# Performance work log

Hardware: AMD Instinct MI355X
Metric: run time of the kernel (lower is better)

## Reference

```python
import jax, jax.numpy as jnp
import numpy as np

HEADS, DIM_HEAD, DIM = 8, 64, 512
INNER = HEADS * DIM_HEAD  # 512


def setup_inputs() -> dict:
    key = jax.random.key(0)
    k1, k2, k3 = jax.random.split(key, 3)
    b, n = 2, 2048
    x = jax.random.normal(k1, (b, n, DIM), dtype=jnp.float32)
    # to_qkv: Linear(dim, 4*inner_dim, bias=False); weight stored [out, in]
    w_qkv = jax.random.normal(k2, (4 * INNER, DIM), dtype=jnp.float32) * (1.0 / np.sqrt(DIM))
    # to_out: Linear(2*inner_dim, dim) with bias
    w_out = jax.random.normal(k3, (DIM, 2 * INNER), dtype=jnp.float32) * (1.0 / np.sqrt(2 * INNER))
    b_out = jnp.zeros((DIM,), dtype=jnp.float32)
    return {"x": x, "w_qkv": w_qkv, "w_out": w_out, "b_out": b_out}


def reference(x, w_qkv, w_out, b_out):
    b, n, d = x.shape
    qkvt = x @ w_qkv.T  # [b, n, 4*inner]
    q, k, v, t = jnp.split(qkvt, 4, axis=-1)

    def split_heads(z):
        return z.reshape(b, n, HEADS, DIM_HEAD).transpose(0, 2, 1, 3)  # [b,h,n,dh]

    q, k, v, t = map(split_heads, (q, k, v, t))

    scale = DIM_HEAD ** -0.5
    dots = jnp.einsum('bhid,bhjd->bhij', q, k) * scale
    attn1 = jax.nn.softmax(dots, axis=-1)

    # fixed positional-decay attention: exp(-|i-j|/e), torch broadcast-normalized
    idx = jnp.arange(1, n + 1, dtype=x.dtype)  # linspace(1, n, n)
    tg = jnp.abs(idx[None, :] - idx[:, None])  # [n, n]
    a2 = jnp.exp(-tg / jnp.exp(jnp.asarray(1.0, x.dtype)))
    a2 = a2 / a2.sum(-1)  # broadcasts over last axis, as in the torch code

    out1 = jnp.einsum('bhij,bhjd->bhid', attn1, v)
    out2 = jnp.einsum('ij,bhjd->bhid', a2, t)
    out = jnp.concatenate([out1, out2], axis=-1)  # [b,h,n,2*dh]
    out = out.transpose(0, 2, 1, 3).reshape(b, n, HEADS * 2 * DIM_HEAD)  # [b,n,2*inner]
    return out @ w_out.T + b_out
```

## Files before the change

### kernel.cpp

```cpp
#include <hip/hip_runtime.h>
#include <hip/hip_bf16.h>
#include <stdint.h>

typedef unsigned short u16;
typedef __bf16 bf16;
typedef __bf16 bf16x8 __attribute__((ext_vector_type(8)));
typedef float f32x4 __attribute__((ext_vector_type(4)));
typedef float f32x16 __attribute__((ext_vector_type(16)));

#define NSEQ 2048
#define NDH 64
#define NH 8
#define QKS 2097152ull

__device__ __forceinline__ float b2f(u16 u) {
  union { float f; uint32_t i; } x; x.i = ((uint32_t)u) << 16; return x.f;
}
__device__ __forceinline__ u16 f2b(float f) {
  union { float f; uint32_t i; } x; x.f = f;
  const uint32_t r = x.i + 0x7FFFu + ((x.i >> 16) & 1u);
  return (u16)(r >> 16);
}
__device__ __forceinline__ uint32_t b2pk(float a, float b) {
  union { __hip_bfloat162 h; uint32_t u; } x;
  x.h = __float22bfloat162_rn(make_float2(a, b));
  return x.u;
}
__device__ __forceinline__ void gl16(const void* g, void* l) {
  __builtin_amdgcn_global_load_lds(
      (const __attribute__((address_space(1))) void*)g,
      (__attribute__((address_space(3))) void*)l, 16, 0, 0);
}

__global__ __launch_bounds__(256) void k_cvt(
    const float* __restrict__ X, const float* __restrict__ Wq,
    const float* __restrict__ Wo, u16* __restrict__ Xb,
    u16* __restrict__ Wqb, u16* __restrict__ Wob) {
  const int b = blockIdx.x;
  const float* src; u16* dst; int idx;
  if (b < 1024)      { src = X;  dst = Xb;  idx = b; }
  else if (b < 1536) { src = Wq; dst = Wqb; idx = b - 1024; }
  else               { src = Wo; dst = Wob; idx = b - 1536; }
  const size_t off = ((size_t)idx * 256 + threadIdx.x) * 8;
  const float4 a = *(const float4*)(src + off);
  const float4 c = *(const float4*)(src + off + 4);
  uint4 o = {b2pk(a.x, a.y), b2pk(a.z, a.w), b2pk(c.x, c.y), b2pk(c.z, c.w)};
  *(uint4*)(dst + off) = o;
}

__global__ __launch_bounds__(256) void k_gemm_qkvt(
    const u16* __restrict__ Xb, const u16* __restrict__ Wb, u16* __restrict__ qkvt) {
  __shared__ __align__(16) bf16 smem[18432];
  bf16* A0e = smem;
  bf16* A1e = smem + 4096;
  bf16* B0e = smem + 8192;
  bf16* B1e = smem + 12288;
  const int tid = threadIdx.x;
  const int m0 = blockIdx.x * 128;
  const int n0 = blockIdx.y * 128;
  const int w = tid >> 6, lane = tid & 63;
  const int wy = w >> 1, wx = w & 1;
  const int quad = lane >> 4, l15 = lane & 15;
  const int srow = tid >> 2, sc8 = (tid & 3) * 8;
  const u16* ag = Xb + (size_t)(m0 + srow) * 512 + sc8;
  const u16* bg = Wb + (size_t)(n0 + srow) * 512 + sc8;
  char* aL00 = (char*)smem + w * 1024;
  char* aL01 = (char*)smem + 4096  + w * 1024;
  char* aL10 = (char*)smem + 8192  + w * 1024;
  char* aL11 = (char*)smem + 12288 + w * 1024;
  char* bL00 = (char*)smem + 16384 + w * 1024;
  char* bL01 = (char*)smem + 20480 + w * 1024;
  char* bL10 = (char*)smem + 24576 + w * 1024;
  char* bL11 = (char*)smem + 28672 + w * 1024;
  f32x4 acc[4][4];
#pragma unroll
  for (int mt = 0; mt < 4; ++mt)
#pragma unroll
    for (int nt = 0; nt < 4; ++nt) acc[mt][nt] = (f32x4){0.f, 0.f, 0.f, 0.f};
  for (int kc = 0; kc < 512; kc += 64) {
    __syncthreads();
    gl16(ag + kc,                 aL00);
    gl16(ag + kc + 64 * 512,      aL01);
    gl16(ag + kc + 32,            aL10);
    gl16(ag + kc + 32 + 64 * 512, aL11);
    gl16(bg + kc,                 bL00);
    gl16(bg + kc + 64 * 512,      bL01);
    gl16(bg + kc + 32,            bL10);
    gl16(bg + kc + 32 + 64 * 512, bL11);
    __syncthreads();
#pragma unroll
    for (int ks = 0; ks < 2; ++ks) {
      const bf16* Ae = ks ? A1e : A0e;
      const bf16* Be = ks ? B1e : B0e;
      bf16x8 afr[4], bfr[4];
#pragma unroll
      for (int mt = 0; mt < 4; ++mt)
        afr[mt] = *(const bf16x8*)&Ae[(wy * 64 + mt * 16 + l15) * 32 + quad * 8];
#pragma unroll
      for (int nt = 0; nt < 4; ++nt)
        bfr[nt] = *(const bf16x8*)&Be[(wx * 64 + nt * 16 + l15) * 32 + quad * 8];
#pragma unroll
      for (int mt = 0; mt < 4; ++mt)
#pragma unroll
        for (int nt = 0; nt < 4; ++nt)
          acc[mt][nt] = __builtin_amdgcn_mfma_f32_16x16x32_bf16(afr[mt], bfr[nt], acc[mt][nt], 0, 0, 0);
    }
  }
  __syncthreads();
  const int cbase = n0 + wx * 64;
  const int which = cbase >> 9;
  const int h     = (cbase >> 6) & 7;
  const float scale = (which == 0) ? 0.18033688011112043f : 1.0f;
  bf16* Cw = smem + w * 4608;
  if (which == 2) {
#pragma unroll
    for (int nt = 0; nt < 4; ++nt)
#pragma unroll
      for (int mt = 0; mt < 4; ++mt)
#pragma unroll
        for (int r = 0; r < 4; ++r)
          Cw[(nt * 16 + l15) * 72 + mt * 16 + quad * 4 + r] = (bf16)acc[mt][nt][r];
  } else {
#pragma unroll
    for (int mt = 0; mt < 4; ++mt)
#pragma unroll
      for (int nt = 0; nt < 4; ++nt)
#pragma unroll
        for (int r = 0; r < 4; ++r)
          Cw[(mt * 16 + quad * 4 + r) * 72 + nt * 16 + l15] = (bf16)(acc[mt][nt][r] * scale);
  }
  const int mb = m0 + wy * 64;
  const int bb = mb >> 11;
  const int nn0 = mb & (NSEQ - 1);
  if (which == 2) {
    u16* vt = qkvt + 2ull * QKS + (size_t)(bb * NH + h) * NDH * NSEQ;
#pragma unroll
    for (int p = 0; p < 8; ++p) {
      const int d = p * 8 + (lane >> 3);
      const int t8 = (lane & 7) * 8;
      const uint4 v = *(const uint4*)&Cw[d * 72 + t8];
      *(uint4*)(vt + (size_t)d * NSEQ + nn0 + t8) = v;
    }
  } else {
    u16* dst = qkvt + (size_t)which * QKS + ((size_t)(bb * NH + h) * NSEQ + nn0) * NDH;
#pragma unroll
    for (int p = 0; p < 8; ++p) {
      const int tok = p * 8 + (lane >> 3);
      const int c8 = (lane & 7) * 8;
      const uint4 v = *(const uint4*)&Cw[tok * 72 + c8];
      *(uint4*)(dst + (size_t)tok * NDH + c8) = v;
    }
  }
}

__global__ __launch_bounds__(256) void k_attn(
    const u16* __restrict__ qkvt, u16* __restrict__ out12) {
  __shared__ float Os[4][32][64];
  __shared__ float Lp[4][32];
  const int tid = threadIdx.x;
  const int bid = blockIdx.x;
  const int bh = bid & 15;
  const int qt = bid >> 4;
  const size_t base  = (size_t)bh * (NSEQ * NDH);
  const size_t vbase = 2ull * QKS + (size_t)bh * (NDH * NSEQ);
  const int wq = tid >> 6, lane = tid & 63;
  const int l31 = lane & 31, hi = lane >> 5;
  const u16* qp = qkvt + base + (size_t)(qt * 32 + l31) * NDH + hi * 8;
  bf16x8 qb[4];
#pragma unroll
  for (int c = 0; c < 4; ++c) qb[c] = *(const bf16x8*)(qp + c * 16);
  const u16* kp = qkvt + QKS + base + (size_t)(wq * 512 + l31) * NDH + hi * 8;
  const u16* vp = qkvt + vbase + (size_t)wq * 512 + hi * 8;
  float lacc = 0.f;
  f32x16 o[2];
#pragma unroll
  for (int nt = 0; nt < 2; ++nt)
#pragma unroll
    for (int r = 0; r < 16; ++r) o[nt][r] = 0.f;
  bf16x8 kf[4];
#pragma unroll
  for (int c = 0; c < 4; ++c) kf[c] = *(const bf16x8*)(kp + c * 16);
  for (int t = 0; t < 16; ++t) {
    bf16x8 vf[2][2];
#pragma unroll
    for (int nt = 0; nt < 2; ++nt)
#pragma unroll
      for (int c = 0; c < 2; ++c)
        vf[nt][c] = *(const bf16x8*)(vp + (size_t)(nt * 32 + l31) * NSEQ + t * 32 + c * 16);
    f32x16 s;
#pragma unroll
    for (int r = 0; r < 16; ++r) s[r] = 0.f;
    __builtin_amdgcn_s_setprio(1);
#pragma unroll
    for (int c = 0; c < 4; ++c)
      s = __builtin_amdgcn_mfma_f32_32x32x16_bf16(kf[c], qb[c], s, 0, 0, 0);
    __builtin_amdgcn_s_setprio(0);
    const int tn = (t + 1) & 15;
    bf16x8 kfn[4];
#pragma unroll
    for (int c = 0; c < 4; ++c)
      kfn[c] = *(const bf16x8*)(kp + (size_t)tn * 32 * NDH + c * 16);
    float ts = 0.f;
#pragma unroll
    for (int r = 0; r < 16; ++r) {
      s[r] = __builtin_amdgcn_exp2f(s[r]);
      ts += s[r];
    }
    ts += __shfl_xor(ts, 32);
    lacc += ts;
    const uint32_t w0 = b2pk(s[0], s[1]),   w1 = b2pk(s[2], s[3]);
    const uint32_t w2 = b2pk(s[4], s[5]),   w3 = b2pk(s[6], s[7]);
    const uint32_t w4 = b2pk(s[8], s[9]),   w5 = b2pk(s[10], s[11]);
    const uint32_t w6 = b2pk(s[12], s[13]), w7 = b2pk(s[14], s[15]);
    const uint32_t e0 = __shfl_xor(hi ? w0 : w2, 32);
    const uint32_t e1 = __shfl_xor(hi ? w1 : w3, 32);
    const uint32_t e2 = __shfl_xor(hi ? w4 : w6, 32);
    const uint32_t e3 = __shfl_xor(hi ? w5 : w7, 32);
    uint4 u0 = hi ? (uint4){e0, e1, w2, w3} : (uint4){w0, w1, e0, e1};
    uint4 u1 = hi ? (uint4){e2, e3, w6, w7} : (uint4){w4, w5, e2, e3};
    const bf16x8 pa0 = *(const bf16x8*)&u0;
    const bf16x8 pa1 = *(const bf16x8*)&u1;
    __builtin_amdgcn_s_setprio(1);
    o[0] = __builtin_amdgcn_mfma_f32_32x32x16_bf16(pa0, vf[0][0], o[0], 0, 0, 0);
    o[0] = __builtin_amdgcn_mfma_f32_32x32x16_bf16(pa1, vf[0][1], o[0], 0, 0, 0);
    o[1] = __builtin_amdgcn_mfma_f32_32x32x16_bf16(pa0, vf[1][0], o[1], 0, 0, 0);
    o[1] = __builtin_amdgcn_mfma_f32_32x32x16_bf16(pa1, vf[1][1], o[1], 0, 0, 0);
    __builtin_amdgcn_s_setprio(0);
#pragma unroll
    for (int c = 0; c < 4; ++c) kf[c] = kfn[c];
  }
#pragma unroll
  for (int nt = 0; nt < 2; ++nt)
#pragma unroll
    for (int r = 0; r < 16; ++r) {
      const int row = (r & 3) + 8 * (r >> 2) + 4 * hi;
      Os[wq][row][nt * 32 + l31] = o[nt][r];
    }
  if (lane < 32) Lp[wq][lane] = lacc;
  __syncthreads();
  const int bb = bh >> 3, h = bh & 7;
#pragma unroll
  for (int rr = 0; rr < 8; ++rr) {
    const int row = wq * 8 + rr;
    const float lt = Lp[0][row] + Lp[1][row] + Lp[2][row] + Lp[3][row];
    const float inv = 1.f / lt;
    const float sum = Os[0][row][lane] + Os[1][row][lane] +
                      Os[2][row][lane] + Os[3][row][lane];
    out12[(size_t)(bb * NSEQ + qt * 32 + row) * 1024 + h * 128 + lane] =
        f2b(sum * inv);
  }
}

__global__ __launch_bounds__(256) void k_band(
    const u16* __restrict__ qkvt, u16* __restrict__ out12) {
  __shared__ float sinv[4][192];
  __shared__ float fbuf[4][64][68];
  const int tid = threadIdx.x;
  const int w = tid >> 6, d = tid & 63;
  const int c  = blockIdx.x * 4 + w;
  const int i0 = c * 64;
  const int bh = blockIdx.y;
  const size_t tb = 3ull * QKS + (size_t)bh * (NSEQ * NDH);
  const float EI = 0.36787944117144233f;
  const float RR = 0.69220062755534635f;
  const float OMR = 1.f - RR;
#pragma unroll
  for (int p = 0; p < 3; ++p) {
    const int j = i0 - 64 + p * 64 + d;
    const float r1 = __expf(-(float)(j + 1) * EI);
    const float r2 = __expf(-(float)(NSEQ - j) * EI);
    sinv[w][p * 64 + d] = OMR / (1.f - r1 + RR - r2);
  }
  const u16* tp = qkvt + tb + d;
  float f = 0.f;
  if (c > 0) {
#pragma unroll 8
    for (int jj = 0; jj < 64; ++jj)
      f = RR * f + sinv[w][jj] * b2f(tp[(size_t)(i0 - 64 + jj) * NDH]);
  }
#pragma unroll 8
  for (int jj = 0; jj < 64; ++jj) {
    f = RR * f + sinv[w][64 + jj] * b2f(tp[(size_t)(i0 + jj) * NDH]);
    fbuf[w][jj][d] = f;
  }
  float b = 0.f;
  if (c < 31) {
#pragma unroll 8
    for (int jj = 63; jj >= 0; --jj)
      b = RR * b + sinv[w][128 + jj] * b2f(tp[(size_t)(i0 + 64 + jj) * NDH]);
  }
  const int bb = bh >> 3, h = bh & 7;
#pragma unroll 8
  for (int jj = 63; jj >= 0; --jj) {
    const float g = sinv[w][64 + jj] * b2f(tp[(size_t)(i0 + jj) * NDH]);
    b = RR * b + g;
    out12[(size_t)(bb * NSEQ + i0 + jj) * 1024 + h * 128 + 64 + d] =
        f2b(fbuf[w][jj][d] + b - g);
  }
}

__global__ __launch_bounds__(256) void k_gemm_out(
    const u16* __restrict__ A, const u16* __restrict__ Wb,
    const float* __restrict__ bias, float* __restrict__ out) {
  __shared__ __align__(16) float smemf[6144];
  bf16* A0e = (bf16*)smemf;
  bf16* A1e = (bf16*)smemf + 4096;
  bf16* B0e = (bf16*)smemf + 8192;
  bf16* B1e = (bf16*)smemf + 10240;
  const int tid = threadIdx.x;
  const int m0 = blockIdx.x * 128;
  const int n0 = blockIdx.y * 64;
  const int w = tid >> 6, lane = tid & 63;
  const int wy = w >> 1, wx = w & 1;
  const int quad = lane >> 4, l15 = lane & 15;
  const int srow = tid >> 2, sc8 = (tid & 3) * 8;
  const u16* ap = A  + (size_t)(m0 + srow) * 1024 + sc8;
  const u16* bp = Wb + (size_t)(n0 + srow) * 1024 + sc8;
  char* aL00 = (char*)smemf + w * 1024;
  char* aL01 = (char*)smemf + 4096  + w * 1024;
  char* aL10 = (char*)smemf + 8192  + w * 1024;
  char* aL11 = (char*)smemf + 12288 + w * 1024;
  char* bL0  = (char*)smemf + 16384 + w * 1024;
  char* bL1  = (char*)smemf + 20480 + w * 1024;
  f32x4 acc[4][2];
#pragma unroll
  for (int mt = 0; mt < 4; ++mt)
#pragma unroll
    for (int nt = 0; nt < 2; ++nt) acc[mt][nt] = (f32x4){0.f, 0.f, 0.f, 0.f};
  for (int kc = 0; kc < 1024; kc += 64) {
    __syncthreads();
    gl16(ap + kc,                  aL00);
    gl16(ap + kc + 64 * 1024,      aL01);
    gl16(ap + kc + 32,             aL10);
    gl16(ap + kc + 32 + 64 * 1024, aL11);
    gl16(bp + kc,                  bL0);
    gl16(bp + kc + 32,             bL1);
    __syncthreads();
#pragma unroll
    for (int ks = 0; ks < 2; ++ks) {
      const bf16* Ae = ks ? A1e : A0e;
      const bf16* Be = ks ? B1e : B0e;
      bf16x8 afr[4], bfr[2];
#pragma unroll
      for (int mt = 0; mt < 4; ++mt)
        afr[mt] = *(const bf16x8*)&Ae[(wy * 64 + mt * 16 + l15) * 32 + quad * 8];
#pragma unroll
      for (int nt = 0; nt < 2; ++nt)
        bfr[nt] = *(const bf16x8*)&Be[(wx * 32 + nt * 16 + l15) * 32 + quad * 8];
#pragma unroll
      for (int mt = 0; mt < 4; ++mt)
#pragma unroll
        for (int nt = 0; nt < 2; ++nt)
          acc[mt][nt] = __builtin_amdgcn_mfma_f32_16x16x32_bf16(afr[mt], bfr[nt], acc[mt][nt], 0, 0, 0);
    }
  }
  float bias_v[2];
#pragma unroll
  for (int nt = 0; nt < 2; ++nt) bias_v[nt] = bias[n0 + wx * 32 + nt * 16 + l15];
  __syncthreads();
  float* Cw = smemf + w * 576;
  const int erow = lane >> 2, ec8 = (lane & 3) * 8;
#pragma unroll
  for (int mt = 0; mt < 4; ++mt) {
#pragma unroll
    for (int nt = 0; nt < 2; ++nt)
#pragma unroll
      for (int r = 0; r < 4; ++r)
        Cw[(quad * 4 + r) * 36 + nt * 16 + l15] = acc[mt][nt][r] + bias_v[nt];
    const float4 v0 = *(const float4*)&Cw[erow * 36 + ec8];
    const float4 v1 = *(const float4*)&Cw[erow * 36 + ec8 + 4];
    float* op = out + (size_t)(m0 + wy * 64 + mt * 16 + erow) * 512 + n0 + wx * 32 + ec8;
    *(float4*)op       = v0;
    *(float4*)(op + 4) = v1;
  }
}

extern "C" void kernel_launch(void* const* d_in, const int* in_sizes, int n_in,
                              void* d_out, int out_size, void* d_ws, size_t ws_size,
                              hipStream_t stream) {
  (void)in_sizes; (void)n_in; (void)out_size; (void)ws_size;
  const float* x     = (const float*)d_in[0];
  const float* w_qkv = (const float*)d_in[1];
  const float* w_out = (const float*)d_in[2];
  const float* b_out = (const float*)d_in[3];
  float* out = (float*)d_out;
  u16* ws    = (u16*)d_ws;
  u16* qkvt  = ws;
  u16* out12 = ws + 8ull  * 1024 * 1024;
  u16* Xb    = ws + 12ull * 1024 * 1024;
  u16* Wqb   = ws + 14ull * 1024 * 1024;
  u16* Wob   = ws + 15ull * 1024 * 1024;
  k_cvt      <<<dim3(1792), 256, 0, stream>>>(x, w_qkv, w_out, Xb, Wqb, Wob);
  k_gemm_qkvt<<<dim3(32, 16), 256, 0, stream>>>(Xb, Wqb, qkvt);
  k_attn     <<<dim3(1024), 256, 0, stream>>>(qkvt, out12);
  k_band     <<<dim3(8, 16), 256, 0, stream>>>(qkvt, out12);
  k_gemm_out <<<dim3(32, 8), 256, 0, stream>>>(out12, Wob, b_out, out);
}
```

Baseline: 176.3 us.

## Stage K and V tiles cooperatively through LDS in attention kernel

New measurement: 281.0 us. +59.4%, slower.

```diff
diff --git a/kernel.cpp b/kernel.cpp
--- a/kernel.cpp
+++ b/kernel.cpp
@@ -153,10 +153,12 @@
   }
 }
 
-__global__ __launch_bounds__(256) void k_attn(
+__global__ __launch_bounds__(256, 4) void k_attn(
     const u16* __restrict__ qkvt, u16* __restrict__ out12) {
-  __shared__ float Os[4][32][64];
-  __shared__ float Lp[4][32];
+  __shared__ __align__(16) char usmem[34816];
+  bf16* Ks = (bf16*)usmem;
+  bf16* Vt = (bf16*)(usmem + 17408);
+  float* Lp = (float*)(usmem + 34304);
   const int tid = threadIdx.x;
   const int bid = blockIdx.x;
   const int bh = bid & 15;
@@ -169,37 +171,49 @@
   bf16x8 qb[4];
 #pragma unroll
   for (int c = 0; c < 4; ++c) qb[c] = *(const bf16x8*)(qp + c * 16);
-  const u16* kp = qkvt + QKS + base + (size_t)(wq * 512 + l31) * NDH + hi * 8;
-  const u16* vp = qkvt + vbase + (size_t)wq * 512 + hi * 8;
+  const int ksrow = tid >> 1, kscol = (tid & 1) * 32;
+  const int vsrow = tid >> 2, vscol = (tid & 3) * 32;
+  const u16* kg = qkvt + QKS + base + (size_t)ksrow * NDH + kscol;
+  const u16* vg = qkvt + vbase + (size_t)vsrow * NSEQ + vscol;
   float lacc = 0.f;
   f32x16 o[2];
 #pragma unroll
   for (int nt = 0; nt < 2; ++nt)
 #pragma unroll
     for (int r = 0; r < 16; ++r) o[nt][r] = 0.f;
-  bf16x8 kf[4];
-#pragma unroll
-  for (int c = 0; c < 4; ++c) kf[c] = *(const bf16x8*)(kp + c * 16);
+  uint4 kr[4], vr[4];
+#pragma unroll
+  for (int i = 0; i < 4; ++i) {
+    kr[i] = *(const uint4*)(kg + i * 8);
+    vr[i] = *(const uint4*)(vg + i * 8);
+  }
   for (int t = 0; t < 16; ++t) {
-    bf16x8 vf[2][2];
-#pragma unroll
-    for (int nt = 0; nt < 2; ++nt)
-#pragma unroll
-      for (int c = 0; c < 2; ++c)
-        vf[nt][c] = *(const bf16x8*)(vp + (size_t)(nt * 32 + l31) * NSEQ + t * 32 + c * 16);
+    __syncthreads();
+#pragma unroll
+    for (int i = 0; i < 4; ++i) {
+      *(uint4*)&Ks[ksrow * 68 + kscol + i * 8] = kr[i];
+      *(uint4*)&Vt[vsrow * 132 + vscol + i * 8] = vr[i];
+    }
+    __syncthreads();
+    if (t < 15) {
+      const u16* kn = kg + (size_t)(t + 1) * 128 * NDH;
+      const u16* vn = vg + (t + 1) * 128;
+#pragma unroll
+      for (int i = 0; i < 4; ++i) {
+        kr[i] = *(const uint4*)(kn + i * 8);
+        vr[i] = *(const uint4*)(vn + i * 8);
+      }
+    }
     f32x16 s;
 #pragma unroll
     for (int r = 0; r < 16; ++r) s[r] = 0.f;
     __builtin_amdgcn_s_setprio(1);
 #pragma unroll
-    for (int c = 0; c < 4; ++c)
-      s = __builtin_amdgcn_mfma_f32_32x32x16_bf16(kf[c], qb[c], s, 0, 0, 0);
+    for (int c = 0; c < 4; ++c) {
+      const bf16x8 ka = *(const bf16x8*)&Ks[(wq * 32 + l31) * 68 + c * 16 + hi * 8];
+      s = __builtin_amdgcn_mfma_f32_32x32x16_bf16(ka, qb[c], s, 0, 0, 0);
+    }
     __builtin_amdgcn_s_setprio(0);
-    const int tn = (t + 1) & 15;
-    bf16x8 kfn[4];
-#pragma unroll
-    for (int c = 0; c < 4; ++c)
-      kfn[c] = *(const bf16x8*)(kp + (size_t)tn * 32 * NDH + c * 16);
     float ts = 0.f;
 #pragma unroll
     for (int r = 0; r < 16; ++r) {
@@ -221,31 +235,34 @@
     const bf16x8 pa0 = *(const bf16x8*)&u0;
     const bf16x8 pa1 = *(const bf16x8*)&u1;
     __builtin_amdgcn_s_setprio(1);
-    o[0] = __builtin_amdgcn_mfma_f32_32x32x16_bf16(pa0, vf[0][0], o[0], 0, 0, 0);
-    o[0] = __builtin_amdgcn_mfma_f32_32x32x16_bf16(pa1, vf[0][1], o[0], 0, 0, 0);
-    o[1] = __builtin_amdgcn_mfma_f32_32x32x16_bf16(pa0, vf[1][0], o[1], 0, 0, 0);
-    o[1] = __builtin_amdgcn_mfma_f32_32x32x16_bf16(pa1, vf[1][1], o[1], 0, 0, 0);
+#pragma unroll
+    for (int nt = 0; nt < 2; ++nt) {
+      const bf16x8 vb0 = *(const bf16x8*)&Vt[(nt * 32 + l31) * 132 + wq * 32 + hi * 8];
+      const bf16x8 vb1 = *(const bf16x8*)&Vt[(nt * 32 + l31) * 132 + wq * 32 + 16 + hi * 8];
+      o[nt] = __builtin_amdgcn_mfma_f32_32x32x16_bf16(pa0, vb0, o[nt], 0, 0, 0);
+      o[nt] = __builtin_amdgcn_mfma_f32_32x32x16_bf16(pa1, vb1, o[nt], 0, 0, 0);
+    }
     __builtin_amdgcn_s_setprio(0);
-#pragma unroll
-    for (int c = 0; c < 4; ++c) kf[c] = kfn[c];
-  }
+  }
+  __syncthreads();
+  float* Os = (float*)usmem;
 #pragma unroll
   for (int nt = 0; nt < 2; ++nt)
 #pragma unroll
     for (int r = 0; r < 16; ++r) {
       const int row = (r & 3) + 8 * (r >> 2) + 4 * hi;
-      Os[wq][row][nt * 32 + l31] = o[nt][r];
-    }
-  if (lane < 32) Lp[wq][lane] = lacc;
+      Os[(wq * 32 + row) * 64 + nt * 32 + l31] = o[nt][r];
+    }
+  if (lane < 32) Lp[wq * 32 + lane] = lacc;
   __syncthreads();
   const int bb = bh >> 3, h = bh & 7;
 #pragma unroll
   for (int rr = 0; rr < 8; ++rr) {
     const int row = wq * 8 + rr;
-    const float lt = Lp[0][row] + Lp[1][row] + Lp[2][row] + Lp[3][row];
+    const float lt = Lp[row] + Lp[32 + row] + Lp[64 + row] + Lp[96 + row];
     const float inv = 1.f / lt;
-    const float sum = Os[0][row][lane] + Os[1][row][lane] +
-                      Os[2][row][lane] + Os[3][row][lane];
+    const float sum = Os[row * 64 + lane] + Os[(32 + row) * 64 + lane] +
+                      Os[(64 + row) * 64 + lane] + Os[(96 + row) * 64 + lane];
     out12[(size_t)(bb * NSEQ + qt * 32 + row) * 1024 + h * 128 + lane] =
         f2b(sum * inv);
   }
```
